# Kernel optimization log

Hardware: AMD Instinct MI355X
Metric: run time of the kernel (lower is better)

Reference implementation:

```python
import jax, jax.numpy as jnp
import numpy as np

B, TED, G, N, E, MD, NOISE = 10000, 512, 64, 2000, 64000, 15, 128
PAC = 10
PACDIM = (TED + NOISE) * PAC  # 6400
D0, D1 = 1024, 512


def _linear_params(k, fan_in, fan_out):
    kw, kb = jax.random.split(k)
    lim = 1.0 / np.sqrt(fan_in)
    w = jax.random.uniform(kw, (fan_in, fan_out), minval=-lim, maxval=lim, dtype=jnp.float32)
    b = jax.random.uniform(kb, (fan_out,), minval=-lim, maxval=lim, dtype=jnp.float32)
    return w, b


def setup_inputs() -> dict:
    key = jax.random.key(0)
    ks = jax.random.split(key, 12)
    inp = {
        'input_': jax.random.normal(ks[0], (B, TED), dtype=jnp.float32),
        'graphs_x': jax.random.normal(ks[1], (G, N, 1), dtype=jnp.float32),
        'edge_index': jax.random.randint(ks[2], (G, 2, E), 0, N, dtype=jnp.int32),
        'graph_ids': jax.random.randint(ks[3], (B,), 0, G, dtype=jnp.int32),
        'chain': jax.random.normal(ks[4], (B, 1), dtype=jnp.float32),
        'metadata': jax.random.normal(ks[5], (B, MD), dtype=jnp.float32),
    }
    inp['gcn_w'], inp['gcn_b'] = _linear_params(ks[6], 1, 1)
    inp['meta_w'], inp['meta_b'] = _linear_params(ks[7], 1 + MD, 32)
    inp['gme_w'], inp['gme_b'] = _linear_params(ks[8], N + 32, NOISE)
    inp['seq_w0'], inp['seq_b0'] = _linear_params(ks[9], PACDIM, D0)
    inp['seq_w1'], inp['seq_b1'] = _linear_params(ks[10], D0, D1)
    inp['seq_w2'], inp['seq_b2'] = _linear_params(ks[11], D1, 1)
    return inp


def _gcn_one(x, ei, gcn_w, gcn_b):
    # GCNConv(1,1) with self-loops and symmetric normalization.
    loops = jnp.arange(N, dtype=ei.dtype)
    src = jnp.concatenate([ei[0], loops])
    dst = jnp.concatenate([ei[1], loops])
    deg = jax.ops.segment_sum(jnp.ones_like(src, dtype=x.dtype), dst, num_segments=N)
    dinv = jax.lax.rsqrt(deg)  # deg >= 1 due to self-loops
    norm = dinv[src] * dinv[dst]  # [E+N]
    xw = x @ gcn_w  # [N,1]
    msg = xw[src] * norm[:, None]
    out = jax.ops.segment_sum(msg, dst, num_segments=N) + gcn_b
    return out.reshape(-1)  # flatten -> [N]


def reference(input_, graphs_x, edge_index, graph_ids, chain, metadata,
              gcn_w, gcn_b, meta_w, meta_b, gme_w, gme_b,
              seq_w0, seq_b0, seq_w1, seq_b1, seq_w2, seq_b2):
    # per-unique-graph GCN, vectorized over G graphs
    gcn_out = jax.vmap(lambda x, ei: _gcn_one(x, ei, gcn_w, gcn_b))(graphs_x, edge_index)  # [G,N]
    graph_emb = gcn_out[graph_ids]  # gather: [B,N]
    all_meta = jnp.concatenate([chain, metadata], axis=1)  # [B,1+MD]
    meta_emb = jax.nn.relu(all_meta @ meta_w + meta_b)  # [B,32]
    noise = jnp.concatenate([graph_emb, meta_emb], axis=1) @ gme_w + gme_b  # [B,NOISE]
    h = jnp.concatenate([input_, noise], axis=1).reshape(-1, PACDIM)  # [B/PAC, PACDIM]
    h = jax.nn.leaky_relu(h @ seq_w0 + seq_b0, 0.2)  # dropout omitted (eval mode)
    h = jax.nn.leaky_relu(h @ seq_w1 + seq_b1, 0.2)
    return h @ seq_w2 + seq_b2  # [B/PAC, 1]
```

## Files before the change

### kernel.cpp

```cpp
#include <hip/hip_runtime.h>

typedef __bf16 bf16_t;
typedef __bf16 bf16x4 __attribute__((ext_vector_type(4)));
typedef __bf16 bf16x8 __attribute__((ext_vector_type(8)));
typedef float floatx4 __attribute__((ext_vector_type(4)));

#define G_GRAPHS 64
#define N_NODES 2000
#define N_EDGES 64000
#define BATCH 10000
#define TED_ 512
#define NOISE_ 128
#define PACDIM_ 6400
#define D0_ 1024
#define D1_ 512
#define MROWS 1000
#define ESPLIT 8
#define EPB (N_EDGES / ESPLIT)
#define MSPLIT 16
#define EPB_MSG (N_EDGES / MSPLIT)
#define S0 8
#define S1 8

__device__ __forceinline__ void glds16(const void* g, void* l) {
    __builtin_amdgcn_global_load_lds(
        (__attribute__((address_space(1))) void*)(g),
        (__attribute__((address_space(3))) void*)(l), 16, 0, 0);
}

__global__ __launch_bounds__(256) void prep_kernel(
    const int* __restrict__ edge_index, float* __restrict__ degs_part,
    const float* __restrict__ in, bf16_t* __restrict__ A,
    const float* __restrict__ W0, bf16_t* __restrict__ W0t,
    const float* __restrict__ W1, bf16_t* __restrict__ W1t)
{
    __shared__ float h[N_NODES];
    __shared__ float t[32][33];
    const int b = blockIdx.x, tid = threadIdx.x;
    if (b < 512) {
        const int s = b & 7, g = b >> 3;
        for (int n = tid; n < N_NODES; n += 256) h[n] = 0.f;
        __syncthreads();
        const int4* d4 = (const int4*)(edge_index + (size_t)g * 2 * N_EDGES
                                       + N_EDGES + s * EPB);
        for (int e = tid; e < EPB / 4; e += 256) {
            int4 v = d4[e];
            atomicAdd(&h[v.x], 1.0f); atomicAdd(&h[v.y], 1.0f);
            atomicAdd(&h[v.z], 1.0f); atomicAdd(&h[v.w], 1.0f);
        }
        __syncthreads();
        float* dp = degs_part + ((size_t)g * ESPLIT + s) * N_NODES;
        for (int n = tid; n < N_NODES; n += 256) dp[n] = h[n];
        return;
    }
    if (b < 5512) {
        int idx = (b - 512) * 256 + tid;
        float4 v = ((const float4*)in)[idx];
        int bb = idx >> 7;
        int c = (idx & 127) << 2;
        int r = bb / 10, slot = bb - r * 10;
        bf16x4 o = { (bf16_t)v.x, (bf16_t)v.y, (bf16_t)v.z, (bf16_t)v.w };
        *(bf16x4*)(A + (size_t)r * PACDIM_ + slot * 640 + c) = o;
        return;
    }
    const float* W; bf16_t* Wt; int Rr, Cc, c0, r0;
    if (b < 11912) {
        int tile = b - 5512;
        W = W0; Wt = W0t; Rr = PACDIM_; Cc = D0_;
        c0 = (tile & 31) << 5; r0 = (tile >> 5) << 5;
    } else {
        int tile = b - 11912;
        W = W1; Wt = W1t; Rr = D0_; Cc = D1_;
        c0 = (tile & 15) << 5; r0 = (tile >> 4) << 5;
    }
    int tx = tid & 31, ty = tid >> 5;
    for (int yy = ty; yy < 32; yy += 8)
        t[yy][tx] = W[(size_t)(r0 + yy) * Cc + c0 + tx];
    __syncthreads();
    for (int yy = ty; yy < 32; yy += 8)
        Wt[(size_t)(c0 + yy) * Rr + r0 + tx] = (bf16_t)t[tx][yy];
}

__global__ __launch_bounds__(512) void msg_kernel(
    const float* __restrict__ graphs_x, const int* __restrict__ edge_index,
    const float* __restrict__ degs_part, float* __restrict__ outs_part)
{
    __shared__ float ys[N_NODES];
    __shared__ float dvl[N_NODES];
    __shared__ float oh[N_NODES];
    const int g = blockIdx.y, s = blockIdx.x, tid = threadIdx.x;
    const float* xg = graphs_x + (size_t)g * N_NODES;
    const float* dgp = degs_part + (size_t)g * ESPLIT * N_NODES;
    for (int n = tid; n < N_NODES; n += 512) {
        float d = 1.0f;
        for (int p = 0; p < ESPLIT; p++) d += dgp[(size_t)p * N_NODES + n];
        float dv = rsqrtf(d);
        dvl[n] = dv;
        ys[n] = xg[n] * dv;
        oh[n] = 0.f;
    }
    __syncthreads();
    const int* src = edge_index + (size_t)g * 2 * N_EDGES + s * EPB_MSG;
    const int2* s2 = (const int2*)src;
    const int2* d2 = (const int2*)(src + N_EDGES);
    for (int e = tid; e < EPB_MSG / 2; e += 512) {
        int2 sv = s2[e], dd = d2[e];
        atomicAdd(&oh[dd.x], ys[sv.x] * dvl[dd.x]);
        atomicAdd(&oh[dd.y], ys[sv.y] * dvl[dd.y]);
    }
    __syncthreads();
    float* op = outs_part + ((size_t)g * MSPLIT + s) * N_NODES;
    for (int n = tid; n < N_NODES; n += 512) op[n] = oh[n];
}

__global__ __launch_bounds__(512) void gnoise_kernel(
    const float* __restrict__ graphs_x, const float* __restrict__ degs_part,
    const float* __restrict__ outs_part,
    const float* __restrict__ gcn_w, const float* __restrict__ gcn_b,
    const float* __restrict__ gme_w, float* __restrict__ gnoise_p)
{
    __shared__ float of[500];
    __shared__ float part[4][128];
    const int s = blockIdx.x, g = blockIdx.y, tid = threadIdx.x;
    const int nBase = s * 500;
    const float w = gcn_w[0], bb = gcn_b[0];
    const float* dgp = degs_part + (size_t)g * ESPLIT * N_NODES;
    const float* otp = outs_part + (size_t)g * MSPLIT * N_NODES;
    for (int n = tid; n < 500; n += 512) {
        int gn = nBase + n;
        float d = 1.0f, o = 0.f;
        for (int p = 0; p < ESPLIT; p++) d += dgp[(size_t)p * N_NODES + gn];
        for (int p = 0; p < MSPLIT; p++) o += otp[(size_t)p * N_NODES + gn];
        of[n] = w * (o + graphs_x[(size_t)g * N_NODES + gn] / d) + bb;
    }
    __syncthreads();
    const int j = tid & 127, ch = tid >> 7;
    float acc = 0.f;
    const int n0 = ch * 125;
    for (int n = n0; n < n0 + 125; n++)
        acc += of[n] * gme_w[(size_t)(nBase + n) * 128 + j];
    part[ch][j] = acc;
    __syncthreads();
    if (tid < 128)
        gnoise_p[((size_t)g * 4 + s) * 128 + tid] =
            part[0][tid] + part[1][tid] + part[2][tid] + part[3][tid];
}

__global__ __launch_bounds__(256) void meta_kernel(
    const float* __restrict__ chain, const float* __restrict__ metadata,
    const int* __restrict__ graph_ids,
    const float* __restrict__ meta_w, const float* __restrict__ meta_b,
    const float* __restrict__ gme_w, const float* __restrict__ gme_b,
    const float* __restrict__ gnoise_p, bf16_t* __restrict__ A)
{
    int wid = (blockIdx.x * 256 + threadIdx.x) >> 6;
    int lane = threadIdx.x & 63;
    if (wid >= BATCH) return;
    const int b = wid;
    float me = 0.f;
    if (lane < 32) {
        me = meta_b[lane] + chain[b] * meta_w[lane];
        for (int i = 1; i < 16; i++)
            me += metadata[(size_t)b * 15 + (i - 1)] * meta_w[(size_t)i * 32 + lane];
        me = me > 0.f ? me : 0.f;
    }
    const int gid = graph_ids[b];
    const float* gp = gnoise_p + (size_t)gid * 4 * 128;
    const int j1 = lane, j2 = lane + 64;
    float n1 = gme_b[j1] + gp[j1] + gp[128 + j1] + gp[256 + j1] + gp[384 + j1];
    float n2 = gme_b[j2] + gp[j2] + gp[128 + j2] + gp[256 + j2] + gp[384 + j2];
    for (int k = 0; k < 32; k++) {
        float mk = __shfl(me, k, 64);
        const float* wrow = gme_w + (size_t)(N_NODES + k) * 128;
        n1 += mk * wrow[j1];
        n2 += mk * wrow[j2];
    }
    int r = b / 10, slot = b - r * 10;
    bf16_t* dp = A + (size_t)r * PACDIM_ + slot * 640 + TED_;
    dp[j1] = (bf16_t)n1;
    dp[j2] = (bf16_t)n2;
}

__global__ __launch_bounds__(256) void gemm_bt_splitk_kernel(
    const bf16_t* __restrict__ A,
    const bf16_t* __restrict__ Bt,
    float* __restrict__ P,
    int M, int N, int K, int KS, int zbits, int xbits, int Mp)
{
    __shared__ __align__(16) bf16_t As[2][128 * 32];
    __shared__ __align__(16) bf16_t Bs[2][128 * 32];
    const int tid = threadIdx.x;
    const int wave = tid >> 6;
    const int lane = tid & 63;
    const int id = blockIdx.x;
    const int z = id & ((1 << zbits) - 1);
    const int xt = (id >> zbits) & ((1 << xbits) - 1);
    const int yt = id >> (zbits + xbits);
    const int mBase = yt * 128;
    const int nBase = xt * 128;
    const int wm = (wave & 1) * 64;
    const int wn = (wave >> 1) * 64;

    floatx4 acc[4][4] = {};

    const int rA0 = tid >> 2;
    const int g4 = tid & 3;
    const int f4 = (rA0 >> 1) & 3;
    const int k8 = (g4 ^ f4) * 8;
    int gm0 = mBase + rA0;      if (gm0 > M - 1) gm0 = M - 1;
    int gm1 = mBase + 64 + rA0; if (gm1 > M - 1) gm1 = M - 1;
    const bf16_t* aP0 = A + (size_t)gm0 * K + k8;
    const bf16_t* aP1 = A + (size_t)gm1 * K + k8;
    const bf16_t* bP0 = Bt + (size_t)(nBase + rA0) * K + k8;
    const bf16_t* bP1 = Bt + (size_t)(nBase + 64 + rA0) * K + k8;

    const int q4 = lane >> 4;
    const int mr = lane & 15;
    const int kq = ((q4 ^ ((mr >> 1) & 3)) * 8);
    int aOff[4], bOff[4];
    for (int i = 0; i < 4; i++) aOff[i] = (wm + i * 16 + mr) * 32 + kq;
    for (int j = 0; j < 4; j++) bOff[j] = (wn + j * 16 + mr) * 32 + kq;

    const int nIter = KS >> 5;
    const int kc = z * KS;
    {
        char* lA = (char*)(&As[0][0]) + wave * 1024;
        char* lB = (char*)(&Bs[0][0]) + wave * 1024;
        glds16(aP0 + kc, lA);
        glds16(aP1 + kc, lA + 4096);
        glds16(bP0 + kc, lB);
        glds16(bP1 + kc, lB + 4096);
    }
    __syncthreads();
    for (int t = 0; t < nIter; ++t) {
        const int cur = t & 1;
        if (t + 1 < nIter) {
            const int kn = kc + (t + 1) * 32;
            char* lA = (char*)(&As[cur ^ 1][0]) + wave * 1024;
            char* lB = (char*)(&Bs[cur ^ 1][0]) + wave * 1024;
            glds16(aP0 + kn, lA);
            glds16(aP1 + kn, lA + 4096);
            glds16(bP0 + kn, lB);
            glds16(bP1 + kn, lB + 4096);
        }
        const bf16_t* aB = &As[cur][0];
        const bf16_t* bB = &Bs[cur][0];
        bf16x8 af[4], bfr[4];
        for (int i = 0; i < 4; i++) af[i] = *(const bf16x8*)(aB + aOff[i]);
        for (int j = 0; j < 4; j++) bfr[j] = *(const bf16x8*)(bB + bOff[j]);
        for (int i = 0; i < 4; i++)
            for (int j = 0; j < 4; j++)
                acc[i][j] = __builtin_amdgcn_mfma_f32_16x16x32_bf16(
                    af[i], bfr[j], acc[i][j], 0, 0, 0);
        __syncthreads();
    }

    float* Pz = P + (size_t)z * Mp * N;
    const int rq = (lane >> 4) * 4;
    const int cn = lane & 15;
    for (int j = 0; j < 4; j++) {
        int col = nBase + wn + j * 16 + cn;
        for (int i = 0; i < 4; i++)
            for (int r = 0; r < 4; r++) {
                int rowm = mBase + wm + i * 16 + rq + r;
                Pz[(size_t)rowm * N + col] = acc[i][j][r];
            }
    }
}

__global__ __launch_bounds__(256) void reduce_bias_leaky_kernel(
    const float* __restrict__ P, const float* __restrict__ bias,
    bf16_t* __restrict__ C, int M, int N, int Mp, int S)
{
    int idx = blockIdx.x * 256 + threadIdx.x;
    int total = M * (N >> 2);
    if (idx >= total) return;
    int nv = N >> 2;
    int r = idx / nv, c4 = (idx - r * nv) << 2;
    size_t off = (size_t)r * N + c4;
    size_t stride = (size_t)Mp * N;
    float4 v = *(const float4*)(P + off);
    for (int s = 1; s < S; s++) {
        float4 u = *(const float4*)(P + s * stride + off);
        v.x += u.x; v.y += u.y; v.z += u.z; v.w += u.w;
    }
    const float4 bv = *(const float4*)(bias + c4);
    v.x += bv.x; v.y += bv.y; v.z += bv.z; v.w += bv.w;
    v.x = v.x > 0.f ? v.x : 0.2f * v.x;
    v.y = v.y > 0.f ? v.y : 0.2f * v.y;
    v.z = v.z > 0.f ? v.z : 0.2f * v.z;
    v.w = v.w > 0.f ? v.w : 0.2f * v.w;
    bf16x4 o = { (bf16_t)v.x, (bf16_t)v.y, (bf16_t)v.z, (bf16_t)v.w };
    *(bf16x4*)(C + off) = o;
}

__global__ __launch_bounds__(256) void final_fused_kernel(
    const float* __restrict__ P, const float* __restrict__ b1,
    const float* __restrict__ w2, const float* __restrict__ b2,
    float* __restrict__ out, int Mp, int S)
{
    int wid = (blockIdx.x * 256 + threadIdx.x) >> 6;
    int lane = threadIdx.x & 63;
    if (wid >= MROWS) return;
    size_t stride = (size_t)Mp * D1_;
    const float* base = P + (size_t)wid * D1_;
    float s = 0.f;
    for (int i = 0; i < 8; i++) {
        int c = i * 64 + lane;
        float v = base[c];
        for (int z = 1; z < S; z++) v += base[(size_t)z * stride + c];
        v += b1[c];
        v = v > 0.f ? v : 0.2f * v;
        s += v * w2[c];
    }
    for (int off = 32; off; off >>= 1) s += __shfl_down(s, off, 64);
    if (lane == 0) out[wid] = s + b2[0];
}

extern "C" void kernel_launch(void* const* d_in, const int* in_sizes, int n_in,
                              void* d_out, int out_size, void* d_ws, size_t ws_size,
                              hipStream_t stream)
{
    const float* input_    = (const float*)d_in[0];
    const float* graphs_x  = (const float*)d_in[1];
    const int*   edge_idx  = (const int*)  d_in[2];
    const int*   graph_ids = (const int*)  d_in[3];
    const float* chain     = (const float*)d_in[4];
    const float* metadata  = (const float*)d_in[5];
    const float* gcn_w     = (const float*)d_in[6];
    const float* gcn_b     = (const float*)d_in[7];
    const float* meta_w    = (const float*)d_in[8];
    const float* meta_b    = (const float*)d_in[9];
    const float* gme_w     = (const float*)d_in[10];
    const float* gme_b     = (const float*)d_in[11];
    const float* seq_w0    = (const float*)d_in[12];
    const float* seq_b0    = (const float*)d_in[13];
    const float* seq_w1    = (const float*)d_in[14];
    const float* seq_b1    = (const float*)d_in[15];
    const float* seq_w2    = (const float*)d_in[16];
    const float* seq_b2    = (const float*)d_in[17];
    float* out = (float*)d_out;

    char* ws = (char*)d_ws;
    float*  degs_part = (float*)(ws + 0);
    float*  outs_part = (float*)(ws + 4096000);
    float*  gnoise_p  = (float*)(ws + 12288000);
    bf16_t* Abuf      = (bf16_t*)(ws + 12419072);
    bf16_t* W0t       = (bf16_t*)(ws + 25219072);
    bf16_t* W1t       = (bf16_t*)(ws + 38326272);
    bf16_t* H1        = (bf16_t*)(ws + 39374848);
    float*  P         = (float*)(ws + 41422848);

    prep_kernel<<<12424, 256, 0, stream>>>(
        edge_idx, degs_part, input_, Abuf, seq_w0, W0t, seq_w1, W1t);
    msg_kernel<<<dim3(MSPLIT, G_GRAPHS), 512, 0, stream>>>(
        graphs_x, edge_idx, degs_part, outs_part);
    gnoise_kernel<<<dim3(4, G_GRAPHS), 512, 0, stream>>>(
        graphs_x, degs_part, outs_part, gcn_w, gcn_b, gme_w, gnoise_p);
    meta_kernel<<<2500, 256, 0, stream>>>(
        chain, metadata, graph_ids, meta_w, meta_b, gme_w, gme_b,
        gnoise_p, Abuf);

    gemm_bt_splitk_kernel<<<512, 256, 0, stream>>>(
        Abuf, W0t, P, MROWS, D0_, PACDIM_, PACDIM_ / S0, 3, 3, 1024);
    reduce_bias_leaky_kernel<<<(MROWS * D0_ / 4 + 255) / 256, 256, 0, stream>>>(
        P, seq_b0, H1, MROWS, D0_, 1024, S0);

    gemm_bt_splitk_kernel<<<256, 256, 0, stream>>>(
        H1, W1t, P, MROWS, D1_, D0_, D0_ / S1, 3, 2, 1024);
    final_fused_kernel<<<(MROWS * 64 + 255) / 256, 256, 0, stream>>>(
        P, seq_b1, seq_w2, seq_b2, out, 1024, S1);
}
```

Measured before the change: 264.2 us.

## Fuse second GEMM with final projection, drop split-K, coarsen prep blocks

Replaces the split-K second GEMM and its separate reduce/final kernel with one kernel that computes the full K=1024 product per 128x128 tile. It then applies bias and leaky-ReLU, dots with w2 and atomically accumulates into the output, which the earlier reduce kernel pre-fills with b2. This removes the partial-sum write/read and one launch, but runs only 32 blocks and makes the output order nondeterministic through atomics. It also halves the message-kernel edge split and makes each input-packing block handle four chunks.

After: 265.1 us. Within noise of the previous version (+0.3%).

```diff
diff --git a/kernel.cpp b/kernel.cpp
--- a/kernel.cpp
+++ b/kernel.cpp
@@ -17,10 +17,14 @@
 #define MROWS 1000
 #define ESPLIT 8
 #define EPB (N_EDGES / ESPLIT)
-#define MSPLIT 16
+#define MSPLIT 8
 #define EPB_MSG (N_EDGES / MSPLIT)
 #define S0 8
-#define S1 8
+
+#define DEG_BLKS 512
+#define PACK_BLKS 1250
+#define W0T_BLKS 6400
+#define W1T_BLKS 512
 
 __device__ __forceinline__ void glds16(const void* g, void* l) {
     __builtin_amdgcn_global_load_lds(
@@ -37,7 +41,7 @@
     __shared__ float h[N_NODES];
     __shared__ float t[32][33];
     const int b = blockIdx.x, tid = threadIdx.x;
-    if (b < 512) {
+    if (b < DEG_BLKS) {
         const int s = b & 7, g = b >> 3;
         for (int n = tid; n < N_NODES; n += 256) h[n] = 0.f;
         __syncthreads();
@@ -53,23 +57,26 @@
         for (int n = tid; n < N_NODES; n += 256) dp[n] = h[n];
         return;
     }
-    if (b < 5512) {
-        int idx = (b - 512) * 256 + tid;
-        float4 v = ((const float4*)in)[idx];
-        int bb = idx >> 7;
-        int c = (idx & 127) << 2;
-        int r = bb / 10, slot = bb - r * 10;
-        bf16x4 o = { (bf16_t)v.x, (bf16_t)v.y, (bf16_t)v.z, (bf16_t)v.w };
-        *(bf16x4*)(A + (size_t)r * PACDIM_ + slot * 640 + c) = o;
+    if (b < DEG_BLKS + PACK_BLKS) {
+        int base = (b - DEG_BLKS) * 1024;
+        for (int u = 0; u < 4; u++) {
+            int idx = base + u * 256 + tid;
+            float4 v = ((const float4*)in)[idx];
+            int bb = idx >> 7;
+            int c = (idx & 127) << 2;
+            int r = bb / 10, slot = bb - r * 10;
+            bf16x4 o = { (bf16_t)v.x, (bf16_t)v.y, (bf16_t)v.z, (bf16_t)v.w };
+            *(bf16x4*)(A + (size_t)r * PACDIM_ + slot * 640 + c) = o;
+        }
         return;
     }
     const float* W; bf16_t* Wt; int Rr, Cc, c0, r0;
-    if (b < 11912) {
-        int tile = b - 5512;
+    if (b < DEG_BLKS + PACK_BLKS + W0T_BLKS) {
+        int tile = b - (DEG_BLKS + PACK_BLKS);
         W = W0; Wt = W0t; Rr = PACDIM_; Cc = D0_;
         c0 = (tile & 31) << 5; r0 = (tile >> 5) << 5;
     } else {
-        int tile = b - 11912;
+        int tile = b - (DEG_BLKS + PACK_BLKS + W0T_BLKS);
         W = W1; Wt = W1t; Rr = D0_; Cc = D1_;
         c0 = (tile & 15) << 5; r0 = (tile >> 4) << 5;
     }
@@ -270,8 +277,13 @@
 
 __global__ __launch_bounds__(256) void reduce_bias_leaky_kernel(
     const float* __restrict__ P, const float* __restrict__ bias,
-    bf16_t* __restrict__ C, int M, int N, int Mp, int S)
-{
+    bf16_t* __restrict__ C, int M, int N, int Mp, int S,
+    const float* __restrict__ b2, float* __restrict__ outp)
+{
+    if (blockIdx.x == 0 && threadIdx.x < MROWS / 4) {
+        float bb2 = b2[0];
+        ((float4*)outp)[threadIdx.x] = make_float4(bb2, bb2, bb2, bb2);
+    }
     int idx = blockIdx.x * 256 + threadIdx.x;
     int total = M * (N >> 2);
     if (idx >= total) return;
@@ -294,27 +306,100 @@
     *(bf16x4*)(C + off) = o;
 }
 
-__global__ __launch_bounds__(256) void final_fused_kernel(
-    const float* __restrict__ P, const float* __restrict__ b1,
-    const float* __restrict__ w2, const float* __restrict__ b2,
-    float* __restrict__ out, int Mp, int S)
-{
-    int wid = (blockIdx.x * 256 + threadIdx.x) >> 6;
-    int lane = threadIdx.x & 63;
-    if (wid >= MROWS) return;
-    size_t stride = (size_t)Mp * D1_;
-    const float* base = P + (size_t)wid * D1_;
-    float s = 0.f;
-    for (int i = 0; i < 8; i++) {
-        int c = i * 64 + lane;
-        float v = base[c];
-        for (int z = 1; z < S; z++) v += base[(size_t)z * stride + c];
-        v += b1[c];
-        v = v > 0.f ? v : 0.2f * v;
-        s += v * w2[c];
-    }
-    for (int off = 32; off; off >>= 1) s += __shfl_down(s, off, 64);
-    if (lane == 0) out[wid] = s + b2[0];
+__global__ __launch_bounds__(256) void gemm1_final_kernel(
+    const bf16_t* __restrict__ A,
+    const bf16_t* __restrict__ Bt,
+    const float* __restrict__ b1, const float* __restrict__ w2,
+    float* __restrict__ outp)
+{
+    __shared__ __align__(16) bf16_t As[2][128 * 32];
+    __shared__ __align__(16) bf16_t Bs[2][128 * 32];
+    const int K = D0_;
+    const int tid = threadIdx.x;
+    const int wave = tid >> 6;
+    const int lane = tid & 63;
+    const int xt = blockIdx.x & 3;
+    const int yt = blockIdx.x >> 2;
+    const int mBase = yt * 128;
+    const int nBase = xt * 128;
+    const int wm = (wave & 1) * 64;
+    const int wn = (wave >> 1) * 64;
+
+    floatx4 acc[4][4] = {};
+
+    const int rA0 = tid >> 2;
+    const int g4 = tid & 3;
+    const int f4 = (rA0 >> 1) & 3;
+    const int k8 = (g4 ^ f4) * 8;
+    int gm0 = mBase + rA0;      if (gm0 > MROWS - 1) gm0 = MROWS - 1;
+    int gm1 = mBase + 64 + rA0; if (gm1 > MROWS - 1) gm1 = MROWS - 1;
+    const bf16_t* aP0 = A + (size_t)gm0 * K + k8;
+    const bf16_t* aP1 = A + (size_t)gm1 * K + k8;
+    const bf16_t* bP0 = Bt + (size_t)(nBase + rA0) * K + k8;
+    const bf16_t* bP1 = Bt + (size_t)(nBase + 64 + rA0) * K + k8;
+
+    const int q4 = lane >> 4;
+    const int mr = lane & 15;
+    const int kq = ((q4 ^ ((mr >> 1) & 3)) * 8);
+    int aOff[4], bOff[4];
+    for (int i = 0; i < 4; i++) aOff[i] = (wm + i * 16 + mr) * 32 + kq;
+    for (int j = 0; j < 4; j++) bOff[j] = (wn + j * 16 + mr) * 32 + kq;
+
+    const int nIter = K >> 5;
+    {
+        char* lA = (char*)(&As[0][0]) + wave * 1024;
+        char* lB = (char*)(&Bs[0][0]) + wave * 1024;
+        glds16(aP0, lA);
+        glds16(aP1, lA + 4096);
+        glds16(bP0, lB);
+        glds16(bP1, lB + 4096);
+    }
+    __syncthreads();
+    for (int t = 0; t < nIter; ++t) {
+        const int cur = t & 1;
+        if (t + 1 < nIter) {
+            const int kn = (t + 1) * 32;
+            char* lA = (char*)(&As[cur ^ 1][0]) + wave * 1024;
+            char* lB = (char*)(&Bs[cur ^ 1][0]) + wave * 1024;
+            glds16(aP0 + kn, lA);
+            glds16(aP1 + kn, lA + 4096);
+            glds16(bP0 + kn, lB);
+            glds16(bP1 + kn, lB + 4096);
+        }
+        const bf16_t* aB = &As[cur][0];
+        const bf16_t* bB = &Bs[cur][0];
+        bf16x8 af[4], bfr[4];
+        for (int i = 0; i < 4; i++) af[i] = *(const bf16x8*)(aB + aOff[i]);
+        for (int j = 0; j < 4; j++) bfr[j] = *(const bf16x8*)(bB + bOff[j]);
+        for (int i = 0; i < 4; i++)
+            for (int j = 0; j < 4; j++)
+                acc[i][j] = __builtin_amdgcn_mfma_f32_16x16x32_bf16(
+                    af[i], bfr[j], acc[i][j], 0, 0, 0);
+        __syncthreads();
+    }
+
+    const int cn = lane & 15;
+    float b1v[4], w2v[4];
+    for (int j = 0; j < 4; j++) {
+        int col = nBase + wn + j * 16 + cn;
+        b1v[j] = b1[col];
+        w2v[j] = w2[col];
+    }
+    for (int i = 0; i < 4; i++) {
+        for (int r = 0; r < 4; r++) {
+            float part = 0.f;
+            for (int j = 0; j < 4; j++) {
+                float v = acc[i][j][r] + b1v[j];
+                v = v > 0.f ? v : 0.2f * v;
+                part += v * w2v[j];
+            }
+            for (int off = 8; off; off >>= 1) part += __shfl_xor(part, off, 16);
+            if (cn == 0) {
+                int rowm = mBase + wm + i * 16 + q4 * 4 + r;
+                if (rowm < MROWS) atomicAdd(&outp[rowm], part);
+            }
+        }
+    }
 }
 
 extern "C" void kernel_launch(void* const* d_in, const int* in_sizes, int n_in,
@@ -344,14 +429,14 @@
     char* ws = (char*)d_ws;
     float*  degs_part = (float*)(ws + 0);
     float*  outs_part = (float*)(ws + 4096000);
-    float*  gnoise_p  = (float*)(ws + 12288000);
-    bf16_t* Abuf      = (bf16_t*)(ws + 12419072);
-    bf16_t* W0t       = (bf16_t*)(ws + 25219072);
-    bf16_t* W1t       = (bf16_t*)(ws + 38326272);
-    bf16_t* H1        = (bf16_t*)(ws + 39374848);
-    float*  P         = (float*)(ws + 41422848);
-
-    prep_kernel<<<12424, 256, 0, stream>>>(
+    float*  gnoise_p  = (float*)(ws + 8192000);
+    bf16_t* Abuf      = (bf16_t*)(ws + 8323072);
+    bf16_t* W0t       = (bf16_t*)(ws + 21123072);
+    bf16_t* W1t       = (bf16_t*)(ws + 34230272);
+    bf16_t* H1        = (bf16_t*)(ws + 35278848);
+    float*  P         = (float*)(ws + 37326848);
+
+    prep_kernel<<<DEG_BLKS + PACK_BLKS + W0T_BLKS + W1T_BLKS, 256, 0, stream>>>(
         edge_idx, degs_part, input_, Abuf, seq_w0, W0t, seq_w1, W1t);
     msg_kernel<<<dim3(MSPLIT, G_GRAPHS), 512, 0, stream>>>(
         graphs_x, edge_idx, degs_part, outs_part);
@@ -364,10 +449,8 @@
     gemm_bt_splitk_kernel<<<512, 256, 0, stream>>>(
         Abuf, W0t, P, MROWS, D0_, PACDIM_, PACDIM_ / S0, 3, 3, 1024);
     reduce_bias_leaky_kernel<<<(MROWS * D0_ / 4 + 255) / 256, 256, 0, stream>>>(
-        P, seq_b0, H1, MROWS, D0_, 1024, S0);
-
-    gemm_bt_splitk_kernel<<<256, 256, 0, stream>>>(
-        H1, W1t, P, MROWS, D1_, D0_, D0_ / S1, 3, 2, 1024);
-    final_fused_kernel<<<(MROWS * 64 + 255) / 256, 256, 0, stream>>>(
-        P, seq_b1, seq_w2, seq_b2, out, 1024, S1);
-}
+        P, seq_b0, H1, MROWS, D0_, 1024, S0, seq_b2, out);
+
+    gemm1_final_kernel<<<32, 256, 0, stream>>>(
+        H1, W1t, seq_b1, seq_w2, out);
+}
```
